# Optimization experiments

Measured on AMD Instinct MI355X. Metric: run time of the kernel, lower is better.

Reference implementation:

```python
import jax, jax.numpy as jnp
import numpy as np

C = 512
REDUCTION = 8
POOLED_LEN = 256


def setup_inputs() -> dict:
    key = jax.random.key(0)
    k_x, k_w1, k_b1, k_w2, k_b2 = jax.random.split(key, 5)
    B, H, W = 32, 64, 64
    hid = C // REDUCTION  # 64
    fan1 = C + POOLED_LEN  # 768
    x = jax.random.normal(k_x, (B, C, H, W), dtype=jnp.float32)
    # torch nn.Linear default init: U(-1/sqrt(fan_in), 1/sqrt(fan_in))
    lim1 = 1.0 / np.sqrt(fan1)
    lim2 = 1.0 / np.sqrt(hid)
    fc1_w = jax.random.uniform(k_w1, (hid, fan1), jnp.float32, -lim1, lim1)
    fc1_b = jax.random.uniform(k_b1, (hid,), jnp.float32, -lim1, lim1)
    fc2_w = jax.random.uniform(k_w2, (1, hid), jnp.float32, -lim2, lim2)
    fc2_b = jax.random.uniform(k_b2, (1,), jnp.float32, -lim2, lim2)
    return {"x": x, "fc1_w": fc1_w, "fc1_b": fc1_b, "fc2_w": fc2_w, "fc2_b": fc2_b}


def reference(x, fc1_w, fc1_b, fc2_w, fc2_b):
    B, Ch, H, W = x.shape
    # spatial mean pool -> channel descriptor [B, C]
    x_c = x.mean(axis=(2, 3))
    # outer-product channel affinity [B, C, C]
    affinity = x_c[:, :, None] * x_c[:, None, :]
    # concat affinity with its transpose along last dim -> [B, C, 2C]
    r_i = jnp.concatenate([affinity, jnp.swapaxes(affinity, 1, 2)], axis=2)
    # adaptive_avg_pool1d(2C -> pooled_len): 2C divisible by pooled_len,
    # so it's exact uniform window averaging
    win = (2 * Ch) // POOLED_LEN
    r_i_pooled = r_i.reshape(B, Ch, POOLED_LEN, win).mean(axis=-1)
    # x_c broadcast along dim 1 -> [B, C, C]
    x_pooled = jnp.broadcast_to(x_c[:, None, :], (B, Ch, Ch))
    att_input = jnp.concatenate([x_pooled, r_i_pooled], axis=2)  # [B, C, C+pooled_len]
    s = jax.nn.relu(jnp.einsum('bcf,hf->bch', att_input, fc1_w) + fc1_b)
    a = jax.nn.sigmoid(jnp.einsum('bch,oh->bco', s, fc2_w) + fc2_b)  # [B, C, 1]
    return x * a[:, :, :, None]  # [B, C, 1, 1] broadcast
```

## Files before the change

kernel.cpp:

```cpp
#include <hip/hip_runtime.h>
#include <math.h>


#define B_  32
#define C_  512
#define HW_ 4096
#define ROWS_ (B_ * C_)

typedef float f32x4 __attribute__((ext_vector_type(4)));

__global__ __launch_bounds__(256) void k_rowmean(const float* __restrict__ x,
                                                 float* __restrict__ xc) {
    const int lane = threadIdx.x & 63;
    const int wave = threadIdx.x >> 6;
    const int row  = blockIdx.x * 4 + wave;
    const f32x4* xr = (const f32x4*)(x + (size_t)row * HW_);
    float s = 0.f;
#pragma unroll
    for (int j = 0; j < 16; ++j) {
        f32x4 v = xr[lane + j * 64];
        s += (v[0] + v[1]) + (v[2] + v[3]);
    }
#pragma unroll
    for (int off = 32; off > 0; off >>= 1) s += __shfl_down(s, off, 64);
    if (lane == 0) xc[row] = s * (1.0f / (float)HW_);
}

__global__ __launch_bounds__(256) void k_att_scale(
        const float* __restrict__ x,
        const float* __restrict__ xc,
        const float* __restrict__ fc1w,
        const float* __restrict__ fc1b,
        const float* __restrict__ fc2w,
        const float* __restrict__ fc2b,
        float* __restrict__ out) {
    const int tid = threadIdx.x;
    const int row_lo = ROWS_ - (int)(blockIdx.x + 1) * 16;
    const int b  = row_lo / C_;
    const int c0 = row_lo % C_;

    __shared__ float xcs[C_];
    __shared__ float qs[128];
    __shared__ float p1[256], p2[256];
    __shared__ float s1[64], s2[64], w2s[64];
    __shared__ float as[16];

    xcs[tid]       = xc[b * C_ + tid];
    xcs[tid + 256] = xc[b * C_ + 256 + tid];
    if (tid < 64) w2s[tid] = fc2w[tid];
    __syncthreads();

    if (tid < 128) {
        qs[tid] = (xcs[4 * tid] + xcs[4 * tid + 1] +
                   xcs[4 * tid + 2] + xcs[4 * tid + 3]) * 0.25f;
    }
    __syncthreads();

    {
        const int h = tid & 63, part = tid >> 6;
        const float* w = fc1w + h * 768;
        float t1 = 0.f, t2 = 0.f;
        const int f0 = part * 128;
#pragma unroll 8
        for (int f = 0; f < 128; ++f) t1 += xcs[f0 + f] * w[f0 + f];
        const int m0 = part * 32;
#pragma unroll 8
        for (int m = 0; m < 32; ++m)
            t2 += qs[m0 + m] * (w[512 + m0 + m] + w[640 + m0 + m]);
        p1[tid] = t1;
        p2[tid] = t2;
    }
    __syncthreads();
    if (tid < 64) {
        s1[tid] = (p1[tid] + p1[tid + 64]) + (p1[tid + 128] + p1[tid + 192]) + fc1b[tid];
        s2[tid] = (p2[tid] + p2[tid + 64]) + (p2[tid + 128] + p2[tid + 192]);
    }
    __syncthreads();

    if (tid < 16) {
        const float xv = xcs[c0 + tid];
        float acc = fc2b[0];
#pragma unroll 8
        for (int hh = 0; hh < 64; ++hh) {
            float z = s1[hh] + xv * s2[hh];
            acc += w2s[hh] * (z > 0.f ? z : 0.f);
        }
        as[tid] = 1.0f / (1.0f + __expf(-acc));
    }
    __syncthreads();

    const int lane = tid & 63, wave = tid >> 6;
#pragma unroll
    for (int r = 0; r < 4; ++r) {
        const int ri  = wave * 4 + r;
        const int row = row_lo + ri;
        const float sc = as[ri];
        const f32x4* xr  = (const f32x4*)(x + (size_t)row * HW_);
        f32x4* outr      = (f32x4*)(out + (size_t)row * HW_);
#pragma unroll
        for (int j = 0; j < 16; ++j) {
            f32x4 v = xr[lane + j * 64];
            v *= sc;
            __builtin_nontemporal_store(v, &outr[lane + j * 64]);
        }
    }
}

extern "C" void kernel_launch(void* const* d_in, const int* in_sizes, int n_in,
                              void* d_out, int out_size, void* d_ws, size_t ws_size,
                              hipStream_t stream) {
    const float* x     = (const float*)d_in[0];
    const float* fc1_w = (const float*)d_in[1];
    const float* fc1_b = (const float*)d_in[2];
    const float* fc2_w = (const float*)d_in[3];
    const float* fc2_b = (const float*)d_in[4];
    float* out = (float*)d_out;

    float* xc = (float*)d_ws;

    k_rowmean<<<ROWS_ / 4, 256, 0, stream>>>(x, xc);
    k_att_scale<<<ROWS_ / 16, 256, 0, stream>>>(x, xc, fc1_w, fc1_b, fc2_w, fc2_b, out);
}
```

Measured before the change: 498.7 us.

## Fuse row-mean and attention-scale kernels with per-batch atomic barrier

Merges the row-mean pass and the attention/scale pass into one kernel. Each block computes means for its 16 rows, then signals a per-batch atomic counter and spins until all 32 blocks of that batch have finished, so it can reread its own rows while they are likely still cache-resident. This removes a kernel launch and the cross-kernel cache eviction, but adds a memset, spin-waiting, and a reliance on all blocks of a batch being co-resident (1024 blocks with launch bounds of 4 per CU) to avoid deadlock.

Result: slower. 865.9 us (+73.6%).

```diff
diff --git a/kernel.cpp b/kernel.cpp
--- a/kernel.cpp
+++ b/kernel.cpp
@@ -6,36 +6,25 @@
 #define C_  512
 #define HW_ 4096
 #define ROWS_ (B_ * C_)
+#define NBLK_ 1024
+#define RPB_  16
+#define BLKS_PER_BATCH_ 32
 
 typedef float f32x4 __attribute__((ext_vector_type(4)));
 
-__global__ __launch_bounds__(256) void k_rowmean(const float* __restrict__ x,
-                                                 float* __restrict__ xc) {
-    const int lane = threadIdx.x & 63;
-    const int wave = threadIdx.x >> 6;
-    const int row  = blockIdx.x * 4 + wave;
-    const f32x4* xr = (const f32x4*)(x + (size_t)row * HW_);
-    float s = 0.f;
-#pragma unroll
-    for (int j = 0; j < 16; ++j) {
-        f32x4 v = xr[lane + j * 64];
-        s += (v[0] + v[1]) + (v[2] + v[3]);
-    }
-#pragma unroll
-    for (int off = 32; off > 0; off >>= 1) s += __shfl_down(s, off, 64);
-    if (lane == 0) xc[row] = s * (1.0f / (float)HW_);
-}
-
-__global__ __launch_bounds__(256) void k_att_scale(
+__global__ __launch_bounds__(256, 4) void fused(
         const float* __restrict__ x,
-        const float* __restrict__ xc,
         const float* __restrict__ fc1w,
         const float* __restrict__ fc1b,
         const float* __restrict__ fc2w,
         const float* __restrict__ fc2b,
-        float* __restrict__ out) {
-    const int tid = threadIdx.x;
-    const int row_lo = ROWS_ - (int)(blockIdx.x + 1) * 16;
+        float* __restrict__ out,
+        float* __restrict__ xc,
+        int* __restrict__ cnt) {
+    const int tid  = threadIdx.x;
+    const int lane = tid & 63;
+    const int wave = tid >> 6;
+    const int row_lo = blockIdx.x * RPB_;
     const int b  = row_lo / C_;
     const int c0 = row_lo % C_;
 
@@ -45,9 +34,37 @@
     __shared__ float s1[64], s2[64], w2s[64];
     __shared__ float as[16];
 
+#pragma unroll
+    for (int r = 0; r < 4; ++r) {
+        const int row = row_lo + wave * 4 + r;
+        const f32x4* xr = (const f32x4*)(x + (size_t)row * HW_);
+        float s = 0.f;
+#pragma unroll
+        for (int j = 0; j < 16; ++j) {
+            f32x4 v = xr[lane + j * 64];
+            s += (v[0] + v[1]) + (v[2] + v[3]);
+        }
+#pragma unroll
+        for (int off = 32; off > 0; off >>= 1) s += __shfl_down(s, off, 64);
+        if (lane == 0) xc[row] = s * (1.0f / (float)HW_);
+    }
+
+    if (tid < 64) w2s[tid] = fc2w[tid];
+
+    __threadfence();
+    __syncthreads();
+    if (tid == 0) {
+        atomicAdd(&cnt[b], 1);
+        while (__hip_atomic_load(&cnt[b], __ATOMIC_ACQUIRE,
+                                 __HIP_MEMORY_SCOPE_AGENT) < BLKS_PER_BATCH_) {
+            __builtin_amdgcn_s_sleep(8);
+        }
+    }
+    __syncthreads();
+    __threadfence();
+
     xcs[tid]       = xc[b * C_ + tid];
     xcs[tid + 256] = xc[b * C_ + 256 + tid];
-    if (tid < 64) w2s[tid] = fc2w[tid];
     __syncthreads();
 
     if (tid < 128) {
@@ -89,14 +106,13 @@
     }
     __syncthreads();
 
-    const int lane = tid & 63, wave = tid >> 6;
 #pragma unroll
     for (int r = 0; r < 4; ++r) {
         const int ri  = wave * 4 + r;
         const int row = row_lo + ri;
         const float sc = as[ri];
-        const f32x4* xr  = (const f32x4*)(x + (size_t)row * HW_);
-        f32x4* outr      = (f32x4*)(out + (size_t)row * HW_);
+        const f32x4* xr = (const f32x4*)(x + (size_t)row * HW_);
+        f32x4* outr     = (f32x4*)(out + (size_t)row * HW_);
 #pragma unroll
         for (int j = 0; j < 16; ++j) {
             f32x4 v = xr[lane + j * 64];
@@ -116,8 +132,9 @@
     const float* fc2_b = (const float*)d_in[4];
     float* out = (float*)d_out;
 
-    float* xc = (float*)d_ws;
+    int*   cnt = (int*)d_ws;
+    float* xc  = (float*)d_ws + 64;
 
-    k_rowmean<<<ROWS_ / 4, 256, 0, stream>>>(x, xc);
-    k_att_scale<<<ROWS_ / 16, 256, 0, stream>>>(x, xc, fc1_w, fc1_b, fc2_w, fc2_b, out);
+    hipMemsetAsync(d_ws, 0, 128, stream);
+    fused<<<NBLK_, 256, 0, stream>>>(x, fc1_w, fc1_b, fc2_w, fc2_b, out, xc, cnt);
 }
```
